# Kernel tuning notes

Hardware: AMD Instinct MI355X
Metric: run time of the kernel (lower is better)

## Reference

```python
import jax, jax.numpy as jnp
import numpy as np

GRID_SIZE = 5
SPLINE_ORDER = 3
GRID_LO, GRID_HI = -1.0, 1.0
N_BASIS = GRID_SIZE + SPLINE_ORDER  # 8


def make_grid():
    # Extended knot vector as in efficient-kan: grid_size+2*spline_order+1 points
    h = (GRID_HI - GRID_LO) / GRID_SIZE
    return (jnp.arange(-SPLINE_ORDER, GRID_SIZE + SPLINE_ORDER + 1, dtype=jnp.float32) * h + GRID_LO)  # (12,)


def b_splines(x, grid):
    # Cox-de Boor recursion; x: (...,) -> (..., N_BASIS)
    xg = x[..., None]
    bases = ((xg >= grid[:-1]) & (xg < grid[1:])).astype(x.dtype)
    for k in range(1, SPLINE_ORDER + 1):
        left = (xg - grid[: -(k + 1)]) / (grid[k:-1] - grid[: -(k + 1)]) * bases[..., :-1]
        right = (grid[k + 1:] - xg) / (grid[k + 1:] - grid[1:-k]) * bases[..., 1:]
        bases = left + right
    return bases


def extract_patches3(x):
    # x: (B, C, H, W) -> (B, C, 9, H, W); 3x3 kernel, stride 1, padding 1
    B, C, H, W = x.shape
    xp = jnp.pad(x, ((0, 0), (0, 0), (1, 1), (1, 1)))
    return jnp.stack([xp[:, :, di:di + H, dj:dj + W]
                      for di in range(3) for dj in range(3)], axis=2)


def kan_conv(x, base_w, spline_w, scaler, grid):
    # One KANLinear(9 -> 1) per (out_ch, in_ch) pair, summed over in_ch.
    p = extract_patches3(x)                          # (B, Cin, 9, H, W)
    base = jnp.einsum('biphw,oip->bohw', jax.nn.silu(p), base_w)
    basis = b_splines(p, grid)                       # (B, Cin, 9, H, W, G)
    sw = spline_w * scaler[..., None]                # standalone spline scaler
    spl = jnp.einsum('biphwg,oipg->bohw', basis, sw)
    return base + spl


def maxpool2(x):
    B, C, H, W = x.shape
    return x.reshape(B, C, H // 2, 2, W // 2, 2).max(axis=(3, 5))


def setup_inputs() -> dict:
    key = jax.random.key(0)
    ks = jax.random.split(key, 7)
    return {
        'x': jax.random.normal(ks[0], (2048, 1, 28, 28), dtype=jnp.float32),
        'base_w1': jax.random.normal(ks[1], (2, 1, 9), dtype=jnp.float32) * 0.3,
        'spline_w1': jax.random.normal(ks[2], (2, 1, 9, 8), dtype=jnp.float32) * 0.1,
        'scaler1': jax.random.normal(ks[3], (2, 1, 9), dtype=jnp.float32) * 0.3 + 1.0,
        'base_w2': jax.random.normal(ks[4], (2, 2, 9), dtype=jnp.float32) * 0.3,
        'spline_w2': jax.random.normal(ks[5], (2, 2, 9, 8), dtype=jnp.float32) * 0.1,
        'scaler2': jax.random.normal(ks[6], (2, 2, 9), dtype=jnp.float32) * 0.3 + 1.0,
    }


def reference(x, base_w1, spline_w1, scaler1, base_w2, spline_w2, scaler2):
    grid = make_grid()
    h = maxpool2(kan_conv(x, base_w1, spline_w1, scaler1, grid))   # (B, 2, 14, 14)
    h = maxpool2(kan_conv(h, base_w2, spline_w2, scaler2, grid))   # (B, 2, 7, 7)
    return h.reshape(h.shape[0], -1)                               # (B, 98)
```

## Files before the change

### kernel.cpp

```cpp
#include <hip/hip_runtime.h>
#include <math.h>

typedef _Float16 half_t;
typedef _Float16 h2 __attribute__((ext_vector_type(2)));
typedef unsigned int uint;
typedef unsigned long long u64;

#define TPB 64

__device__ __forceinline__ uint pack_h2f(float a, float b) {
  half_t ha = (half_t)a, hb = (half_t)b;
  unsigned short ua = __builtin_bit_cast(unsigned short, ha);
  unsigned short ub = __builtin_bit_cast(unsigned short, hb);
  return (uint)ua | ((uint)ub << 16);
}

__device__ __forceinline__ float silu_f(float x) {
  float e = __expf(-x);
  return x * __builtin_amdgcn_rcpf(1.0f + e);
}

__device__ __forceinline__ float dot8(uint d0, uint d1, uint d2, uint d3,
                                      float sv, const uint* __restrict__ w,
                                      float acc) {
  acc = fmaf(sv, __uint_as_float(w[4]), acc);
#if __has_builtin(__builtin_amdgcn_fdot2)
  acc = __builtin_amdgcn_fdot2(__builtin_bit_cast(h2, d0), __builtin_bit_cast(h2, w[0]), acc, false);
  acc = __builtin_amdgcn_fdot2(__builtin_bit_cast(h2, d1), __builtin_bit_cast(h2, w[1]), acc, false);
  acc = __builtin_amdgcn_fdot2(__builtin_bit_cast(h2, d2), __builtin_bit_cast(h2, w[2]), acc, false);
  acc = __builtin_amdgcn_fdot2(__builtin_bit_cast(h2, d3), __builtin_bit_cast(h2, w[3]), acc, false);
#else
  uint dd[4] = {d0, d1, d2, d3};
#pragma unroll
  for (int k = 0; k < 4; ++k) {
    h2 f = __builtin_bit_cast(h2, dd[k]);
    h2 wv = __builtin_bit_cast(h2, w[k]);
    acc = fmaf((float)f.x, (float)wv.x, acc);
    acc = fmaf((float)f.y, (float)wv.y, acc);
  }
#endif
  return acc;
}

__device__ __forceinline__ uint4 make_basis(float x) {
  float s = fmaf(x, 2.5f, 5.5f);
  float sf = floorf(s);
  float t = s - sf;
  int p = (int)sf - 3;
  float omt = 1.0f - t, t2 = t * t;
  float B0 = (1.0f / 6.0f) * omt * omt * omt;
  float B3 = (1.0f / 6.0f) * t2 * t;
  float B1 = fmaf(0.5f * t, t2, 2.0f / 3.0f - t2);
  float B2 = 1.0f - B0 - B1 - B3;
  u64 A = ((u64)pack_h2f(B2, B3) << 32) | pack_h2f(B0, B1);
  int n = p < 0 ? -p : 0;
  A = (n >= 4) ? 0ull : (A >> (16 * n));
  int pc = p < 0 ? 0 : (p > 9 ? 9 : p);
  int sh = 16 * pc;
  u64 lo = (sh < 64) ? (A << sh) : 0ull;
  u64 hi = (sh == 0) ? 0ull
         : (sh < 64) ? (A >> (64 - sh))
         : (sh < 128) ? (A << (sh - 64)) : 0ull;
  return make_uint4((uint)lo, (uint)(lo >> 32), (uint)hi, (uint)(hi >> 32));
}

__global__ void pack_w(const float* __restrict__ bw1, const float* __restrict__ sw1,
                       const float* __restrict__ sc1, const float* __restrict__ bw2,
                       const float* __restrict__ sw2, const float* __restrict__ sc2,
                       uint* __restrict__ W) {
  const int t = threadIdx.x;
  if (t < 18) {
    const float scv = sc1[t];
    uint* dst = W + t * 5;
#pragma unroll
    for (int j = 0; j < 4; ++j)
      dst[j] = pack_h2f(sw1[t * 8 + 2 * j] * scv, sw1[t * 8 + 2 * j + 1] * scv);
    dst[4] = __float_as_uint(bw1[t]);
  } else if (t < 54) {
    const int q = t - 18;
    const float scv = sc2[q];
    uint* dst = W + 90 + q * 5;
#pragma unroll
    for (int j = 0; j < 4; ++j)
      dst[j] = pack_h2f(sw2[q * 8 + 2 * j] * scv, sw2[q * 8 + 2 * j + 1] * scv);
    dst[4] = __float_as_uint(bw2[q]);
  }
}

#define F2DB 3136
#define F2SB 4704

__global__ __launch_bounds__(TPB, 2) void kan_fwd(
    const float* __restrict__ x, const uint* __restrict__ W,
    float* __restrict__ out)
{
  __shared__ __align__(16) uint lds[4900];
  half_t* F2S = (half_t*)&lds[F2SB];

  const int lane = threadIdx.x;
  const float* xb = x + (size_t)blockIdx.x * 784;

  const uint F0d1 = pack_h2f(1.0f / 48.0f, 23.0f / 48.0f);
  const uint F0d2 = pack_h2f(23.0f / 48.0f, 1.0f / 48.0f);

  for (int s = lane; s < 784; s += TPB) {
    uint4 bs = make_basis(xb[s]);
    *(uint4*)&lds[s * 4] = bs;
  }
  __syncthreads();

  for (int k = 0; k < 4; ++k) {
    const int q = lane + 64 * k;
    if (q < 196) {
      const int ph = q / 14, pw = q - (q / 14) * 14;
      float acc[2][4];
#pragma unroll
      for (int o = 0; o < 2; ++o)
#pragma unroll
        for (int j = 0; j < 4; ++j) acc[o][j] = 0.0f;
#pragma unroll
      for (int r = 0; r < 4; ++r) {
        const int ir = 2 * ph + r - 1;
#pragma unroll
        for (int c = 0; c < 4; ++c) {
          const int ic = 2 * pw + c - 1;
          const bool ok = ((uint)ir < 28u) && ((uint)ic < 28u);
          const int idx = min(max(ir * 28 + ic, 0), 783);
          float xv = xb[idx];
          const float sv = ok ? silu_f(xv) : 0.0f;
          const uint4 d = *(const uint4*)&lds[idx * 4];
          const uint d0 = ok ? d.x : 0u;
          const uint d1 = ok ? d.y : F0d1;
          const uint d2 = ok ? d.z : F0d2;
          const uint d3 = ok ? d.w : 0u;
#pragma unroll
          for (int dh = 0; dh < 2; ++dh) {
            if (r - dh < 0 || r - dh > 2) continue;
#pragma unroll
            for (int dw = 0; dw < 2; ++dw) {
              if (c - dw < 0 || c - dw > 2) continue;
              const int tap = (r - dh) * 3 + (c - dw);
#pragma unroll
              for (int o = 0; o < 2; ++o)
                acc[o][dh * 2 + dw] =
                    dot8(d0, d1, d2, d3, sv, W + (o * 9 + tap) * 5, acc[o][dh * 2 + dw]);
            }
          }
        }
      }
#pragma unroll
      for (int o = 0; o < 2; ++o) {
        const float m = fmaxf(fmaxf(acc[o][0], acc[o][1]), fmaxf(acc[o][2], acc[o][3]));
        const int fi = o * 196 + q;
        uint4 bm = make_basis(m);
        *(uint4*)&lds[F2DB + fi * 4] = bm;
        F2S[fi] = (half_t)silu_f(m);
      }
    }
  }
  __syncthreads();

  if (lane < 49) {
    const int ph = lane / 7, pw = lane - (lane / 7) * 7;
    float pa[2][4];
#pragma unroll
    for (int o = 0; o < 2; ++o)
#pragma unroll
      for (int j = 0; j < 4; ++j) pa[o][j] = 0.0f;
#pragma unroll
    for (int ci = 0; ci < 2; ++ci) {
#pragma unroll
      for (int r = 0; r < 4; ++r) {
        const int row = 2 * ph + r - 1;
        const int rcl = min(max(row, 0), 13);
#pragma unroll
        for (int c = 0; c < 4; ++c) {
          const int col = 2 * pw + c - 1;
          const bool ok = ((uint)row < 14u) && ((uint)col < 14u);
          const int ccl = min(max(col, 0), 13);
          const int idx = ci * 196 + rcl * 14 + ccl;
          const uint4 d = *(const uint4*)&lds[F2DB + idx * 4];
          float sv = (float)F2S[idx];
          sv = ok ? sv : 0.0f;
          const uint d0 = ok ? d.x : 0u;
          const uint d1 = ok ? d.y : F0d1;
          const uint d2 = ok ? d.z : F0d2;
          const uint d3 = ok ? d.w : 0u;
#pragma unroll
          for (int dh = 0; dh < 2; ++dh) {
            if (r - dh < 0 || r - dh > 2) continue;
#pragma unroll
            for (int dw = 0; dw < 2; ++dw) {
              if (c - dw < 0 || c - dw > 2) continue;
              const int tap = (r - dh) * 3 + (c - dw);
#pragma unroll
              for (int o = 0; o < 2; ++o)
                pa[o][dh * 2 + dw] =
                    dot8(d0, d1, d2, d3, sv,
                         W + 90 + ((o * 2 + ci) * 9 + tap) * 5, pa[o][dh * 2 + dw]);
            }
          }
        }
      }
    }
#pragma unroll
    for (int o = 0; o < 2; ++o) {
      const float m = fmaxf(fmaxf(pa[o][0], pa[o][1]), fmaxf(pa[o][2], pa[o][3]));
      out[(size_t)blockIdx.x * 98 + o * 49 + lane] = m;
    }
  }
}

extern "C" void kernel_launch(void* const* d_in, const int* in_sizes, int n_in,
                              void* d_out, int out_size, void* d_ws, size_t ws_size,
                              hipStream_t stream) {
  const float* x   = (const float*)d_in[0];
  const float* bw1 = (const float*)d_in[1];
  const float* sw1 = (const float*)d_in[2];
  const float* sc1 = (const float*)d_in[3];
  const float* bw2 = (const float*)d_in[4];
  const float* sw2 = (const float*)d_in[5];
  const float* sc2 = (const float*)d_in[6];
  float* out = (float*)d_out;
  uint* W = (uint*)d_ws;
  const int B = in_sizes[0] / 784;
  pack_w<<<1, 64, 0, stream>>>(bw1, sw1, sc1, bw2, sw2, sc2, W);
  kan_fwd<<<B, TPB, 0, stream>>>(x, W, out);
}
```

Before: 97.09 us.

## Widen block to 256 threads and split layer-2 work across waves

```diff
diff --git a/kernel.cpp b/kernel.cpp
--- a/kernel.cpp
+++ b/kernel.cpp
@@ -6,7 +6,7 @@
 typedef unsigned int uint;
 typedef unsigned long long u64;
 
-#define TPB 64
+#define TPB 256
 
 __device__ __forceinline__ uint pack_h2f(float a, float b) {
   half_t ha = (half_t)a, hb = (half_t)b;
@@ -90,85 +90,81 @@
 #define F2DB 3136
 #define F2SB 4704
 
-__global__ __launch_bounds__(TPB, 2) void kan_fwd(
+__global__ __launch_bounds__(TPB, 8) void kan_fwd(
     const float* __restrict__ x, const uint* __restrict__ W,
     float* __restrict__ out)
 {
   __shared__ __align__(16) uint lds[4900];
   half_t* F2S = (half_t*)&lds[F2SB];
-
-  const int lane = threadIdx.x;
+  float* P = (float*)lds;
+
+  const int tid = threadIdx.x;
   const float* xb = x + (size_t)blockIdx.x * 784;
 
   const uint F0d1 = pack_h2f(1.0f / 48.0f, 23.0f / 48.0f);
   const uint F0d2 = pack_h2f(23.0f / 48.0f, 1.0f / 48.0f);
 
-  for (int s = lane; s < 784; s += TPB) {
+  for (int s = tid; s < 784; s += TPB) {
     uint4 bs = make_basis(xb[s]);
     *(uint4*)&lds[s * 4] = bs;
   }
   __syncthreads();
 
-  for (int k = 0; k < 4; ++k) {
-    const int q = lane + 64 * k;
-    if (q < 196) {
-      const int ph = q / 14, pw = q - (q / 14) * 14;
-      float acc[2][4];
-#pragma unroll
-      for (int o = 0; o < 2; ++o)
-#pragma unroll
-        for (int j = 0; j < 4; ++j) acc[o][j] = 0.0f;
-#pragma unroll
-      for (int r = 0; r < 4; ++r) {
-        const int ir = 2 * ph + r - 1;
-#pragma unroll
-        for (int c = 0; c < 4; ++c) {
-          const int ic = 2 * pw + c - 1;
-          const bool ok = ((uint)ir < 28u) && ((uint)ic < 28u);
-          const int idx = min(max(ir * 28 + ic, 0), 783);
-          float xv = xb[idx];
-          const float sv = ok ? silu_f(xv) : 0.0f;
-          const uint4 d = *(const uint4*)&lds[idx * 4];
-          const uint d0 = ok ? d.x : 0u;
-          const uint d1 = ok ? d.y : F0d1;
-          const uint d2 = ok ? d.z : F0d2;
-          const uint d3 = ok ? d.w : 0u;
-#pragma unroll
-          for (int dh = 0; dh < 2; ++dh) {
-            if (r - dh < 0 || r - dh > 2) continue;
-#pragma unroll
-            for (int dw = 0; dw < 2; ++dw) {
-              if (c - dw < 0 || c - dw > 2) continue;
-              const int tap = (r - dh) * 3 + (c - dw);
-#pragma unroll
-              for (int o = 0; o < 2; ++o)
-                acc[o][dh * 2 + dw] =
-                    dot8(d0, d1, d2, d3, sv, W + (o * 9 + tap) * 5, acc[o][dh * 2 + dw]);
-            }
+  if (tid < 196) {
+    const int ph = tid / 14, pw = tid % 14;
+    float acc[2][4];
+#pragma unroll
+    for (int o = 0; o < 2; ++o)
+#pragma unroll
+      for (int q = 0; q < 4; ++q) acc[o][q] = 0.0f;
+#pragma unroll
+    for (int r = 0; r < 4; ++r) {
+      const int ir = 2 * ph + r - 1;
+#pragma unroll
+      for (int c = 0; c < 4; ++c) {
+        const int ic = 2 * pw + c - 1;
+        const bool ok = ((uint)ir < 28u) && ((uint)ic < 28u);
+        const int idx = min(max(ir * 28 + ic, 0), 783);
+        const float xv = xb[idx];
+        const float sv = ok ? silu_f(xv) : 0.0f;
+        const uint4 d = *(const uint4*)&lds[idx * 4];
+        const uint d0 = ok ? d.x : 0u;
+        const uint d1 = ok ? d.y : F0d1;
+        const uint d2 = ok ? d.z : F0d2;
+        const uint d3 = ok ? d.w : 0u;
+#pragma unroll
+        for (int dh = 0; dh < 2; ++dh) {
+          if (r - dh < 0 || r - dh > 2) continue;
+#pragma unroll
+          for (int dw = 0; dw < 2; ++dw) {
+            if (c - dw < 0 || c - dw > 2) continue;
+            const int tap = (r - dh) * 3 + (c - dw);
+#pragma unroll
+            for (int o = 0; o < 2; ++o)
+              acc[o][dh * 2 + dw] =
+                  dot8(d0, d1, d2, d3, sv, W + (o * 9 + tap) * 5, acc[o][dh * 2 + dw]);
           }
         }
       }
-#pragma unroll
-      for (int o = 0; o < 2; ++o) {
-        const float m = fmaxf(fmaxf(acc[o][0], acc[o][1]), fmaxf(acc[o][2], acc[o][3]));
-        const int fi = o * 196 + q;
-        uint4 bm = make_basis(m);
-        *(uint4*)&lds[F2DB + fi * 4] = bm;
-        F2S[fi] = (half_t)silu_f(m);
-      }
     }
+#pragma unroll
+    for (int o = 0; o < 2; ++o) {
+      float m = fmaxf(fmaxf(acc[o][0], acc[o][1]), fmaxf(acc[o][2], acc[o][3]));
+      const int fi = o * 196 + tid;
+      uint4 bm = make_basis(m);
+      *(uint4*)&lds[F2DB + fi * 4] = bm;
+      F2S[fi] = (half_t)silu_f(m);
+    }
   }
   __syncthreads();
 
-  if (lane < 49) {
-    const int ph = lane / 7, pw = lane - (lane / 7) * 7;
-    float pa[2][4];
-#pragma unroll
-    for (int o = 0; o < 2; ++o)
-#pragma unroll
-      for (int j = 0; j < 4; ++j) pa[o][j] = 0.0f;
-#pragma unroll
-    for (int ci = 0; ci < 2; ++ci) {
+  {
+    const int wid = __builtin_amdgcn_readfirstlane(tid >> 6);
+    const int lane = tid & 63;
+    if (lane < 49) {
+      const int ci = wid & 1;
+      const int ph = lane / 7, pw = lane % 7;
+      float pa[4] = {0.0f, 0.0f, 0.0f, 0.0f};
 #pragma unroll
       for (int r = 0; r < 4; ++r) {
         const int row = 2 * ph + r - 1;
@@ -193,21 +189,23 @@
             for (int dw = 0; dw < 2; ++dw) {
               if (c - dw < 0 || c - dw > 2) continue;
               const int tap = (r - dh) * 3 + (c - dw);
-#pragma unroll
-              for (int o = 0; o < 2; ++o)
-                pa[o][dh * 2 + dw] =
-                    dot8(d0, d1, d2, d3, sv,
-                         W + 90 + ((o * 2 + ci) * 9 + tap) * 5, pa[o][dh * 2 + dw]);
+              pa[dh * 2 + dw] =
+                  dot8(d0, d1, d2, d3, sv, W + 90 + (wid * 9 + tap) * 5, pa[dh * 2 + dw]);
             }
           }
         }
       }
+      *(float4*)&P[(wid * 49 + lane) * 4] = make_float4(pa[0], pa[1], pa[2], pa[3]);
     }
-#pragma unroll
-    for (int o = 0; o < 2; ++o) {
-      const float m = fmaxf(fmaxf(pa[o][0], pa[o][1]), fmaxf(pa[o][2], pa[o][3]));
-      out[(size_t)blockIdx.x * 98 + o * 49 + lane] = m;
-    }
+  }
+  __syncthreads();
+
+  if (tid < 98) {
+    const int o = tid / 49, pos = tid % 49;
+    const float4 p0 = *(const float4*)&P[((o * 2 + 0) * 49 + pos) * 4];
+    const float4 p1 = *(const float4*)&P[((o * 2 + 1) * 49 + pos) * 4];
+    float m = fmaxf(fmaxf(p0.x + p1.x, p0.y + p1.y), fmaxf(p0.z + p1.z, p0.w + p1.w));
+    out[(size_t)blockIdx.x * 98 + tid] = m;
   }
 }
 
```

Measured after the change: 159.1 us. 1.64x slower.
